# Optimization experiments

Hardware: AMD Instinct MI355X
Metric: run time of the kernel (lower is better)

Reference implementation:

```python
import jax, jax.numpy as jnp
import numpy as np

T, B = 512, 64
DIM_INPUT, DIM_LATENT, VOCAB = 512, 1024, 50257


def setup_inputs() -> dict:
    key = jax.random.key(0)
    ks = jax.random.split(key, 12)
    s = 0.02
    return {
        "X": jax.random.randint(ks[0], (T, B), 0, VOCAB, dtype=jnp.int32),
        "h": jax.random.normal(ks[1], (B, DIM_LATENT), dtype=jnp.float32),
        "emb": jax.random.normal(ks[2], (VOCAB, DIM_INPUT), dtype=jnp.float32) * s,
        "Wf": jax.random.normal(ks[3], (DIM_LATENT + DIM_INPUT, DIM_LATENT), dtype=jnp.float32) * s,
        "bf": jnp.zeros((DIM_LATENT,), dtype=jnp.float32),
        "Wi": jax.random.normal(ks[4], (DIM_LATENT + DIM_INPUT, DIM_LATENT), dtype=jnp.float32) * s,
        "bi": jnp.zeros((DIM_LATENT,), dtype=jnp.float32),
        "Wc": jax.random.normal(ks[5], (DIM_LATENT + DIM_INPUT, DIM_LATENT), dtype=jnp.float32) * s,
        "bc": jnp.zeros((DIM_LATENT,), dtype=jnp.float32),
        "Wo": jax.random.normal(ks[6], (DIM_LATENT + DIM_INPUT, DIM_LATENT), dtype=jnp.float32) * s,
        "bo": jnp.zeros((DIM_LATENT,), dtype=jnp.float32),
    }


def reference(X, h, emb, Wf, bf, Wi, bi, Wc, bc, Wo, bo):
    # X: [T, B] int tokens; h: [B, dim_latent]
    xe = emb[X]  # [T, B, dim_input] embedding gather
    c0 = jnp.zeros_like(h)

    def step(carry, x_t):
        h_prev, c_prev = carry
        m = jnp.concatenate([h_prev, x_t], axis=1)  # [B, dl+di]
        ft = jax.nn.sigmoid(m @ Wf + bf)
        it = jax.nn.sigmoid(m @ Wi + bi)
        ct = ft * c_prev + it * jnp.tanh(m @ Wc + bc)
        ot = jax.nn.sigmoid(m @ Wo + bo)
        ht = ot * jnp.tanh(ct)
        return (ht, ct), ht

    (_, _), H = jax.lax.scan(step, (h, c0), xe)
    return H  # [T, B, dim_latent]
```

## Files before the change

### kernel.cpp

```cpp
#include <hip/hip_runtime.h>


namespace {
constexpr int T_STEPS = 512;
constexpr int BATCH   = 64;
constexpr int DI      = 512;
constexpr int DL      = 1024;
constexpr int NKC     = 48;
constexpr int NKC_H   = 32;
constexpr int NBLK    = 256;
constexpr int NTHR    = 256;
constexpr int FPAD    = 32;
}

typedef __attribute__((ext_vector_type(8))) short bf16x8;
typedef __attribute__((ext_vector_type(8))) unsigned short u16x8;
typedef __attribute__((ext_vector_type(4))) float f32x4;
typedef __attribute__((ext_vector_type(4))) unsigned int u32x4;
typedef __attribute__((ext_vector_type(2))) unsigned int u32x2;

__device__ __forceinline__ unsigned short f2bf(float x){
  unsigned int u = __float_as_uint(x);
  return (unsigned short)((u + 0x7FFFu + ((u >> 16) & 1u)) >> 16);
}
__device__ __forceinline__ float bf2f(unsigned short b){
  return __uint_as_float(((unsigned int)b) << 16);
}
__device__ __forceinline__ float fast_sigmoid(float v){
  return __fdividef(1.f, 1.f + __expf(-v));
}
__device__ __forceinline__ float fast_tanh(float v){
  v = fminf(fmaxf(v, -15.f), 15.f);
  float t = __expf(2.f * v);
  return __fdividef(t - 1.f, t + 1.f);
}

__global__ void prep_xe(const int* __restrict__ X, const float* __restrict__ emb,
                        unsigned short* __restrict__ xe){
  int i = blockIdx.x * blockDim.x + threadIdx.x;
  const int total = T_STEPS * BATCH * DI / 8;
  if (i >= total) return;
  int row = i >> 6;
  int seg = i & 63;
  int tok = X[row];
  const float* src = emb + (long long)tok * DI + seg * 8;
  float4 v0 = *(const float4*)src;
  float4 v1 = *(const float4*)(src + 4);
  u16x8 o;
  o[0]=f2bf(v0.x); o[1]=f2bf(v0.y); o[2]=f2bf(v0.z); o[3]=f2bf(v0.w);
  o[4]=f2bf(v1.x); o[5]=f2bf(v1.y); o[6]=f2bf(v1.z); o[7]=f2bf(v1.w);
  *(u16x8*)(xe + (long long)row * DI + seg * 8) = o;
}

__global__ void prep_w(const float* __restrict__ Wf, const float* __restrict__ Wi,
                       const float* __restrict__ Wc, const float* __restrict__ Wo,
                       unsigned short* __restrict__ W_hi, unsigned short* __restrict__ W_lo){
  int idx = blockIdx.x * blockDim.x + threadIdx.x;
  if (idx >= 256 * NKC * 64) return;
  int lane = idx & 63;
  int kc   = (idx >> 6) % NKC;
  int bk   = idx / (64 * NKC);
  int lc = lane & 15, kg = lane >> 4;
  int g  = lc >> 2;
  int jl = bk * 4 + (lc & 3);
  const float* Wg = (g == 0) ? Wf : ((g == 1) ? Wi : ((g == 2) ? Wc : Wo));
  int kbase = kc * 32 + kg * 8;
  u16x8 hi, lo;
#pragma unroll
  for (int j = 0; j < 8; j++){
    float wv = Wg[(long long)(kbase + j) * DL + jl];
    unsigned short h = f2bf(wv);
    hi[j] = h;
    lo[j] = f2bf(wv - bf2f(h));
  }
  *(u16x8*)(W_hi + ((long long)(bk * NKC + kc) * 64 + lane) * 8) = hi;
  if (kc < NKC_H)
    *(u16x8*)(W_lo + ((long long)(bk * NKC_H + kc) * 64 + lane) * 8) = lo;
}

__global__ void prep_h(const float* __restrict__ h0,
                       const float* __restrict__ bf_, const float* __restrict__ bi_,
                       const float* __restrict__ bc_, const float* __restrict__ bo_,
                       unsigned short* __restrict__ hRing,
                       float* __restrict__ bias_pack, unsigned int* __restrict__ bar){
  int i = blockIdx.x * blockDim.x + threadIdx.x;
  if (i < BATCH * DL) hRing[i] = f2bf(h0[i]);
  if (i < 4096){
    int r = i & 3, g = (i >> 2) & 3, bk = i >> 4;
    const float* bg = (g == 0) ? bf_ : ((g == 1) ? bi_ : ((g == 2) ? bc_ : bo_));
    bias_pack[i] = bg[bk * 4 + r];
  }
  if (i < 8 * FPAD) bar[i] = 0u;
}

template<bool CACHED>
__launch_bounds__(NTHR, 1)
__global__ void lstm_persist(const unsigned short* __restrict__ xe,
                             const unsigned short* __restrict__ W_hi,
                             const unsigned short* __restrict__ W_lo,
                             unsigned short* __restrict__ hRing,
                             const float* __restrict__ bias_pack,
                             float* __restrict__ out,
                             unsigned int* __restrict__ bar){
  extern __shared__ unsigned short lds[];
  unsigned short* lds_hi = lds;
  unsigned short* lds_lo = lds + NKC * 512;
  __shared__ unsigned short stage_h[BATCH * 4];
  __shared__ float          stage_o[BATCH * 4];
  const int tid  = threadIdx.x;
  const int bk   = blockIdx.x;
  const int w    = tid >> 6;
  const int lane = tid & 63;

  const uint4* srcHi = (const uint4*)(W_hi + (size_t)bk * NKC * 512);
  uint4* dHi = (uint4*)lds_hi;
  for (int i = tid; i < 3072; i += NTHR) dHi[i] = srcHi[i];
  const uint4* srcLo = (const uint4*)(W_lo + (size_t)bk * NKC_H * 512);
  uint4* dLo = (uint4*)lds_lo;
  for (int i = tid; i < 2048; i += NTHR) dLo[i] = srcLo[i];
  __syncthreads();

  const int lc = lane & 15;
  const int kg = lane >> 4;
  const int g  = lc >> 2;
  const int rowb = (w << 4) + lc;
  const float bias = bias_pack[bk * 16 + lc];
  const int srcBase = (lane & 48) | (lc & 3);
  const int hOff = rowb * DL + kg * 8;
  const int xOff = rowb * DI + kg * 8;
  float cr0 = 0.f, cr1 = 0.f, cr2 = 0.f, cr3 = 0.f;

  f32x4 acc0 = {0.f,0.f,0.f,0.f}, acc1 = {0.f,0.f,0.f,0.f};
  f32x4 acc2 = {0.f,0.f,0.f,0.f}, acc3 = {0.f,0.f,0.f,0.f};

#define XSTEP(KC, ACC) {                                                        \
    bf16x8 ax = *(const bf16x8*)(xRow + (KC) * 32);                             \
    bf16x8 bh = *(const bf16x8*)(lds_hi + (NKC_H + (KC)) * 512 + lane * 8);     \
    ACC = __builtin_amdgcn_mfma_f32_16x16x32_bf16(ax, bh, ACC, 0, 0, 0); }
#define HSTEP2(KC, ACC) {                                                       \
    bf16x8 ah = *(const bf16x8*)&hv[KC];                                        \
    bf16x8 bh = *(const bf16x8*)(lds_hi + (KC) * 512 + lane * 8);               \
    bf16x8 bl = *(const bf16x8*)(lds_lo + (KC) * 512 + lane * 8);               \
    ACC = __builtin_amdgcn_mfma_f32_16x16x32_bf16(ah, bh, ACC, 0, 0, 0);        \
    ACC = __builtin_amdgcn_mfma_f32_16x16x32_bf16(ah, bl, ACC, 0, 0, 0); }
#define LOADHC(I, OFFSTR)                                                       \
    asm volatile("global_load_dwordx4 %0, %1, off offset:" OFFSTR               \
                 : "=v"(hv[I]) : "v"(hbase));
#define LOADHU(I, OFFSTR)                                                       \
    asm volatile("global_load_dwordx4 %0, %1, off offset:" OFFSTR " sc0 sc1"    \
                 : "=v"(hv[I]) : "v"(hbase));

  {
    const unsigned short* xRow = xe + xOff;
#pragma unroll
    for (int kc = 0; kc < 16; kc += 4){
      XSTEP(kc, acc0) XSTEP(kc + 1, acc1) XSTEP(kc + 2, acc2) XSTEP(kc + 3, acc3)
    }
  }

#pragma unroll 1
  for (int t = 0; t < T_STEPS; ++t){
    if (t > 0 && w == 0){
      const unsigned tgt = (unsigned)NBLK * (unsigned)t;
      int spin = 0;
      while (__hip_atomic_load(bar, __ATOMIC_RELAXED, __HIP_MEMORY_SCOPE_AGENT) < tgt){
        __builtin_amdgcn_s_sleep(1);
        if (++spin > (1 << 16)) break;
      }
    }
    __syncthreads();

    const int slotR = CACHED ? t       : (t & 1);
    const int slotW = CACHED ? (t + 1) : ((t + 1) & 1);
    unsigned short* hWr = hRing + (size_t)slotW * (BATCH * DL);
    float* out_t = out + (size_t)t * (BATCH * DL);

    u32x4 hv[32];
    const unsigned short* hbase = hRing + (size_t)slotR * (BATCH * DL) + hOff;
    if constexpr (CACHED){
      LOADHC( 0,"0")    LOADHC( 1,"64")   LOADHC( 2,"128")  LOADHC( 3,"192")
      LOADHC( 4,"256")  LOADHC( 5,"320")  LOADHC( 6,"384")  LOADHC( 7,"448")
      LOADHC( 8,"512")  LOADHC( 9,"576")  LOADHC(10,"640")  LOADHC(11,"704")
      LOADHC(12,"768")  LOADHC(13,"832")  LOADHC(14,"896")  LOADHC(15,"960")
      LOADHC(16,"1024") LOADHC(17,"1088") LOADHC(18,"1152") LOADHC(19,"1216")
      LOADHC(20,"1280") LOADHC(21,"1344") LOADHC(22,"1408") LOADHC(23,"1472")
      LOADHC(24,"1536") LOADHC(25,"1600") LOADHC(26,"1664") LOADHC(27,"1728")
      LOADHC(28,"1792") LOADHC(29,"1856") LOADHC(30,"1920") LOADHC(31,"1984")
    } else {
      LOADHU( 0,"0")    LOADHU( 1,"64")   LOADHU( 2,"128")  LOADHU( 3,"192")
      LOADHU( 4,"256")  LOADHU( 5,"320")  LOADHU( 6,"384")  LOADHU( 7,"448")
      LOADHU( 8,"512")  LOADHU( 9,"576")  LOADHU(10,"640")  LOADHU(11,"704")
      LOADHU(12,"768")  LOADHU(13,"832")  LOADHU(14,"896")  LOADHU(15,"960")
      LOADHU(16,"1024") LOADHU(17,"1088") LOADHU(18,"1152") LOADHU(19,"1216")
      LOADHU(20,"1280") LOADHU(21,"1344") LOADHU(22,"1408") LOADHU(23,"1472")
      LOADHU(24,"1536") LOADHU(25,"1600") LOADHU(26,"1664") LOADHU(27,"1728")
      LOADHU(28,"1792") LOADHU(29,"1856") LOADHU(30,"1920") LOADHU(31,"1984")
    }
    asm volatile("s_waitcnt vmcnt(0)" ::: "memory");
    __builtin_amdgcn_sched_barrier(0);

#pragma unroll
    for (int kc = 0; kc < NKC_H; kc += 4){
      HSTEP2(kc, acc0) HSTEP2(kc + 1, acc1) HSTEP2(kc + 2, acc2) HSTEP2(kc + 3, acc3)
    }
    f32x4 acc = (acc0 + acc1) + (acc2 + acc3);

    float creg[4] = {cr0, cr1, cr2, cr3};
#pragma unroll
    for (int r = 0; r < 4; r++){
      float v = acc[r] + bias;
      float vF = __shfl(v, srcBase);
      float vI = __shfl(v, srcBase + 4);
      float vC = __shfl(v, srcBase + 8);
      float vO = __shfl(v, srcBase + 12);
      if (g == 0){
        int b = (w << 4) | (kg << 2) | r;
        float ft = fast_sigmoid(vF);
        float it = fast_sigmoid(vI);
        float gt = fast_tanh(vC);
        float ot = fast_sigmoid(vO);
        float cn = ft * creg[r] + it * gt;
        creg[r] = cn;
        float hn = ot * fast_tanh(cn);
        int si = (b << 2) | (lc & 3);
        stage_h[si] = f2bf(hn);
        stage_o[si] = hn;
      }
    }
    cr0 = creg[0]; cr1 = creg[1]; cr2 = creg[2]; cr3 = creg[3];

    __syncthreads();

    if (w == 0){
      u32x2  hv2 = *(const u32x2*)&stage_h[lane << 2];
      f32x4  ov  = *(const f32x4*)&stage_o[lane << 2];
      *(float4*)(out_t + lane * DL + (bk << 2)) = *(const float4*)&ov;
      unsigned short* hdst = hWr + lane * DL + (bk << 2);
      asm volatile("global_store_dwordx2 %0, %1, off sc0 sc1"
                   :: "v"(hdst), "v"(hv2) : "memory");
      asm volatile("s_waitcnt vmcnt(0)" ::: "memory");
      __builtin_amdgcn_sched_barrier(0);
      if (tid == 0)
        __hip_atomic_fetch_add(bar, 1u, __ATOMIC_RELAXED, __HIP_MEMORY_SCOPE_AGENT);
    }

    acc0 = (f32x4){0.f,0.f,0.f,0.f}; acc1 = (f32x4){0.f,0.f,0.f,0.f};
    acc2 = (f32x4){0.f,0.f,0.f,0.f}; acc3 = (f32x4){0.f,0.f,0.f,0.f};
    if (t + 1 < T_STEPS){
      const unsigned short* xRow = xe + (size_t)(t + 1) * BATCH * DI + xOff;
#pragma unroll
      for (int kc = 0; kc < 16; kc += 4){
        XSTEP(kc, acc0) XSTEP(kc + 1, acc1) XSTEP(kc + 2, acc2) XSTEP(kc + 3, acc3)
      }
    }
  }
#undef XSTEP
#undef HSTEP2
#undef LOADHC
#undef LOADHU
}

extern "C" void kernel_launch(void* const* d_in, const int* in_sizes, int n_in,
                              void* d_out, int out_size, void* d_ws, size_t ws_size,
                              hipStream_t stream){
  const int*   X   = (const int*)d_in[0];
  const float* h0  = (const float*)d_in[1];
  const float* emb = (const float*)d_in[2];
  const float* Wf  = (const float*)d_in[3];
  const float* bf_ = (const float*)d_in[4];
  const float* Wi  = (const float*)d_in[5];
  const float* bi_ = (const float*)d_in[6];
  const float* Wc  = (const float*)d_in[7];
  const float* bc_ = (const float*)d_in[8];
  const float* Wo  = (const float*)d_in[9];
  const float* bo_ = (const float*)d_in[10];
  float* out = (float*)d_out;

  const size_t SLOT = (size_t)BATCH * DL;
  const size_t base_need =
      sizeof(unsigned short) * ((size_t)T_STEPS * BATCH * DI
                              + (size_t)256 * NKC * 512
                              + (size_t)256 * NKC_H * 512)
    + sizeof(float) * 4096
    + sizeof(unsigned int) * 8 * FPAD + 4096;
  const size_t ring_full = sizeof(unsigned short) * SLOT * (size_t)(T_STEPS + 1);
  const bool cached = ws_size >= base_need + ring_full;
  const size_t ring_elems = cached ? SLOT * (size_t)(T_STEPS + 1) : SLOT * 2;

  char* ws = (char*)d_ws;
  size_t off = 0;
  auto alloc = [&](size_t bytes) -> void* {
    void* p = ws + off;
    off = (off + bytes + 255) & ~((size_t)255);
    return p;
  };
  unsigned short* xe        = (unsigned short*)alloc(sizeof(unsigned short) * (size_t)T_STEPS * BATCH * DI);
  unsigned short* W_hi      = (unsigned short*)alloc(sizeof(unsigned short) * (size_t)256 * NKC * 512);
  unsigned short* W_lo      = (unsigned short*)alloc(sizeof(unsigned short) * (size_t)256 * NKC_H * 512);
  unsigned short* hRing     = (unsigned short*)alloc(sizeof(unsigned short) * ring_elems);
  float*          bias_pack = (float*)alloc(sizeof(float) * 4096);
  unsigned int*   bar       = (unsigned int*)alloc(sizeof(unsigned int) * 8 * FPAD);
  (void)in_sizes; (void)n_in; (void)out_size;

  static bool attr_set = false;
  if (!attr_set){
    hipFuncSetAttribute((const void*)lstm_persist<true>,
                        hipFuncAttributeMaxDynamicSharedMemorySize, 160 * 1024);
    hipFuncSetAttribute((const void*)lstm_persist<false>,
                        hipFuncAttributeMaxDynamicSharedMemorySize, 160 * 1024);
    attr_set = true;
  }

  hipLaunchKernelGGL(prep_xe, dim3(8192), dim3(256), 0, stream, X, emb, xe);
  hipLaunchKernelGGL(prep_w,  dim3(3072), dim3(256), 0, stream, Wf, Wi, Wc, Wo, W_hi, W_lo);
  hipLaunchKernelGGL(prep_h,  dim3(256),  dim3(256), 0, stream, h0, bf_, bi_, bc_, bo_,
                     hRing, bias_pack, bar);
  if (cached)
    hipLaunchKernelGGL((lstm_persist<true>),  dim3(NBLK), dim3(NTHR), 80 * 1024, stream,
                       xe, W_hi, W_lo, hRing, bias_pack, out, bar);
  else
    hipLaunchKernelGGL((lstm_persist<false>), dim3(NBLK), dim3(NTHR), 80 * 1024, stream,
                       xe, W_hi, W_lo, hRing, bias_pack, out, bar);
}
```

Measured before the change: 4.905 ms.

## Replace global atomic barrier with sentinel-polled h ring for step sync

The per-step global atomic counter barrier and the block-wide syncthreads are replaced by dataflow synchronization. The whole h ring is pre-filled with a sentinel value, and each wave issues its h loads for the next step early, then re-polls only the chunks that still hold sentinel values until valid data arrives. Each wave now writes its own outputs directly instead of staging them through wave 0. This removes the all-block barrier latency and lets waves proceed as soon as their data is ready. In exchange it adds a full-ring fill kernel, requires a full-length ring in the workspace with no fallback, relies on torn 16-byte visibility being caught by a partial sentinel check, and uses a spin cap that could silently read stale data.

After: 8.863 ms. +80.7%, slower.

```diff
diff --git a/kernel.cpp b/kernel.cpp
--- a/kernel.cpp
+++ b/kernel.cpp
@@ -10,7 +10,7 @@
 constexpr int NKC_H   = 32;
 constexpr int NBLK    = 256;
 constexpr int NTHR    = 256;
-constexpr int FPAD    = 32;
+constexpr unsigned SENT = 0xFFFFFFFFu;
 }
 
 typedef __attribute__((ext_vector_type(8))) short bf16x8;
@@ -33,6 +33,11 @@
   v = fminf(fmaxf(v, -15.f), 15.f);
   float t = __expf(2.f * v);
   return __fdividef(t - 1.f, t + 1.f);
+}
+
+__global__ void prep_ring(u32x4* __restrict__ dst, int n16){
+  int i = blockIdx.x * blockDim.x + threadIdx.x;
+  if (i < n16) dst[i] = (u32x4){SENT, SENT, SENT, SENT};
 }
 
 __global__ void prep_xe(const int* __restrict__ X, const float* __restrict__ emb,
@@ -82,7 +87,7 @@
                        const float* __restrict__ bf_, const float* __restrict__ bi_,
                        const float* __restrict__ bc_, const float* __restrict__ bo_,
                        unsigned short* __restrict__ hRing,
-                       float* __restrict__ bias_pack, unsigned int* __restrict__ bar){
+                       float* __restrict__ bias_pack){
   int i = blockIdx.x * blockDim.x + threadIdx.x;
   if (i < BATCH * DL) hRing[i] = f2bf(h0[i]);
   if (i < 4096){
@@ -90,23 +95,20 @@
     const float* bg = (g == 0) ? bf_ : ((g == 1) ? bi_ : ((g == 2) ? bc_ : bo_));
     bias_pack[i] = bg[bk * 4 + r];
   }
-  if (i < 8 * FPAD) bar[i] = 0u;
-}
-
-template<bool CACHED>
+}
+
 __launch_bounds__(NTHR, 1)
 __global__ void lstm_persist(const unsigned short* __restrict__ xe,
                              const unsigned short* __restrict__ W_hi,
                              const unsigned short* __restrict__ W_lo,
                              unsigned short* __restrict__ hRing,
                              const float* __restrict__ bias_pack,
-                             float* __restrict__ out,
-                             unsigned int* __restrict__ bar){
+                             float* __restrict__ out){
   extern __shared__ unsigned short lds[];
   unsigned short* lds_hi = lds;
   unsigned short* lds_lo = lds + NKC * 512;
-  __shared__ unsigned short stage_h[BATCH * 4];
-  __shared__ float          stage_o[BATCH * 4];
+  __shared__ __align__(8)  unsigned short sh_h[4][64];
+  __shared__ __align__(16) float          sh_o[4][64];
   const int tid  = threadIdx.x;
   const int bk   = blockIdx.x;
   const int w    = tid >> 6;
@@ -132,6 +134,7 @@
 
   f32x4 acc0 = {0.f,0.f,0.f,0.f}, acc1 = {0.f,0.f,0.f,0.f};
   f32x4 acc2 = {0.f,0.f,0.f,0.f}, acc3 = {0.f,0.f,0.f,0.f};
+  u32x4 hv[32];
 
 #define XSTEP(KC, ACC) {                                                        \
     bf16x8 ax = *(const bf16x8*)(xRow + (KC) * 32);                             \
@@ -143,14 +146,28 @@
     bf16x8 bl = *(const bf16x8*)(lds_lo + (KC) * 512 + lane * 8);               \
     ACC = __builtin_amdgcn_mfma_f32_16x16x32_bf16(ah, bh, ACC, 0, 0, 0);        \
     ACC = __builtin_amdgcn_mfma_f32_16x16x32_bf16(ah, bl, ACC, 0, 0, 0); }
-#define LOADHC(I, OFFSTR)                                                       \
-    asm volatile("global_load_dwordx4 %0, %1, off offset:" OFFSTR               \
-                 : "=v"(hv[I]) : "v"(hbase));
 #define LOADHU(I, OFFSTR)                                                       \
     asm volatile("global_load_dwordx4 %0, %1, off offset:" OFFSTR " sc0 sc1"    \
                  : "=v"(hv[I]) : "v"(hbase));
+#define ISSUE_ALL                                                               \
+    LOADHU( 0,"0")    LOADHU( 1,"64")   LOADHU( 2,"128")  LOADHU( 3,"192")     \
+    LOADHU( 4,"256")  LOADHU( 5,"320")  LOADHU( 6,"384")  LOADHU( 7,"448")     \
+    LOADHU( 8,"512")  LOADHU( 9,"576")  LOADHU(10,"640")  LOADHU(11,"704")     \
+    LOADHU(12,"768")  LOADHU(13,"832")  LOADHU(14,"896")  LOADHU(15,"960")     \
+    LOADHU(16,"1024") LOADHU(17,"1088") LOADHU(18,"1152") LOADHU(19,"1216")    \
+    LOADHU(20,"1280") LOADHU(21,"1344") LOADHU(22,"1408") LOADHU(23,"1472")    \
+    LOADHU(24,"1536") LOADHU(25,"1600") LOADHU(26,"1664") LOADHU(27,"1728")    \
+    LOADHU(28,"1792") LOADHU(29,"1856") LOADHU(30,"1920") LOADHU(31,"1984")
+#define CHK(KC) { int bad = (hv[KC][0] == SENT) | (hv[KC][2] == SENT);          \
+                  if (__any(bad)) inval |= (1u << (KC)); }
+#define RLD(KC, OFFSTR) if (inval & (1u << (KC))) { LOADHU(KC, OFFSTR) }
+#define RCK(KC) if (inval & (1u << (KC))) {                                     \
+                  int bad = (hv[KC][0] == SENT) | (hv[KC][2] == SENT);          \
+                  if (!__any(bad)) inval &= ~(1u << (KC)); }
 
   {
+    const unsigned short* hbase = hRing + hOff;
+    ISSUE_ALL
     const unsigned short* xRow = xe + xOff;
 #pragma unroll
     for (int kc = 0; kc < 16; kc += 4){
@@ -160,44 +177,35 @@
 
 #pragma unroll 1
   for (int t = 0; t < T_STEPS; ++t){
-    if (t > 0 && w == 0){
-      const unsigned tgt = (unsigned)NBLK * (unsigned)t;
-      int spin = 0;
-      while (__hip_atomic_load(bar, __ATOMIC_RELAXED, __HIP_MEMORY_SCOPE_AGENT) < tgt){
-        __builtin_amdgcn_s_sleep(1);
-        if (++spin > (1 << 16)) break;
-      }
-    }
-    __syncthreads();
-
-    const int slotR = CACHED ? t       : (t & 1);
-    const int slotW = CACHED ? (t + 1) : ((t + 1) & 1);
-    unsigned short* hWr = hRing + (size_t)slotW * (BATCH * DL);
-    float* out_t = out + (size_t)t * (BATCH * DL);
-
-    u32x4 hv[32];
-    const unsigned short* hbase = hRing + (size_t)slotR * (BATCH * DL) + hOff;
-    if constexpr (CACHED){
-      LOADHC( 0,"0")    LOADHC( 1,"64")   LOADHC( 2,"128")  LOADHC( 3,"192")
-      LOADHC( 4,"256")  LOADHC( 5,"320")  LOADHC( 6,"384")  LOADHC( 7,"448")
-      LOADHC( 8,"512")  LOADHC( 9,"576")  LOADHC(10,"640")  LOADHC(11,"704")
-      LOADHC(12,"768")  LOADHC(13,"832")  LOADHC(14,"896")  LOADHC(15,"960")
-      LOADHC(16,"1024") LOADHC(17,"1088") LOADHC(18,"1152") LOADHC(19,"1216")
-      LOADHC(20,"1280") LOADHC(21,"1344") LOADHC(22,"1408") LOADHC(23,"1472")
-      LOADHC(24,"1536") LOADHC(25,"1600") LOADHC(26,"1664") LOADHC(27,"1728")
-      LOADHC(28,"1792") LOADHC(29,"1856") LOADHC(30,"1920") LOADHC(31,"1984")
-    } else {
-      LOADHU( 0,"0")    LOADHU( 1,"64")   LOADHU( 2,"128")  LOADHU( 3,"192")
-      LOADHU( 4,"256")  LOADHU( 5,"320")  LOADHU( 6,"384")  LOADHU( 7,"448")
-      LOADHU( 8,"512")  LOADHU( 9,"576")  LOADHU(10,"640")  LOADHU(11,"704")
-      LOADHU(12,"768")  LOADHU(13,"832")  LOADHU(14,"896")  LOADHU(15,"960")
-      LOADHU(16,"1024") LOADHU(17,"1088") LOADHU(18,"1152") LOADHU(19,"1216")
-      LOADHU(20,"1280") LOADHU(21,"1344") LOADHU(22,"1408") LOADHU(23,"1472")
-      LOADHU(24,"1536") LOADHU(25,"1600") LOADHU(26,"1664") LOADHU(27,"1728")
-      LOADHU(28,"1792") LOADHU(29,"1856") LOADHU(30,"1920") LOADHU(31,"1984")
-    }
     asm volatile("s_waitcnt vmcnt(0)" ::: "memory");
     __builtin_amdgcn_sched_barrier(0);
+    unsigned inval = 0u;
+    CHK( 0) CHK( 1) CHK( 2) CHK( 3) CHK( 4) CHK( 5) CHK( 6) CHK( 7)
+    CHK( 8) CHK( 9) CHK(10) CHK(11) CHK(12) CHK(13) CHK(14) CHK(15)
+    CHK(16) CHK(17) CHK(18) CHK(19) CHK(20) CHK(21) CHK(22) CHK(23)
+    CHK(24) CHK(25) CHK(26) CHK(27) CHK(28) CHK(29) CHK(30) CHK(31)
+    if (inval){
+      const unsigned short* hbase = hRing + (size_t)t * (BATCH * DL) + hOff;
+      int spin = 0;
+      do {
+        __builtin_amdgcn_s_sleep(1);
+        RLD( 0,"0")    RLD( 1,"64")   RLD( 2,"128")  RLD( 3,"192")
+        RLD( 4,"256")  RLD( 5,"320")  RLD( 6,"384")  RLD( 7,"448")
+        RLD( 8,"512")  RLD( 9,"576")  RLD(10,"640")  RLD(11,"704")
+        RLD(12,"768")  RLD(13,"832")  RLD(14,"896")  RLD(15,"960")
+        RLD(16,"1024") RLD(17,"1088") RLD(18,"1152") RLD(19,"1216")
+        RLD(20,"1280") RLD(21,"1344") RLD(22,"1408") RLD(23,"1472")
+        RLD(24,"1536") RLD(25,"1600") RLD(26,"1664") RLD(27,"1728")
+        RLD(28,"1792") RLD(29,"1856") RLD(30,"1920") RLD(31,"1984")
+        asm volatile("s_waitcnt vmcnt(0)" ::: "memory");
+        __builtin_amdgcn_sched_barrier(0);
+        RCK( 0) RCK( 1) RCK( 2) RCK( 3) RCK( 4) RCK( 5) RCK( 6) RCK( 7)
+        RCK( 8) RCK( 9) RCK(10) RCK(11) RCK(12) RCK(13) RCK(14) RCK(15)
+        RCK(16) RCK(17) RCK(18) RCK(19) RCK(20) RCK(21) RCK(22) RCK(23)
+        RCK(24) RCK(25) RCK(26) RCK(27) RCK(28) RCK(29) RCK(30) RCK(31)
+        if (++spin > (1 << 15)) break;
+      } while (inval);
+    }
 
 #pragma unroll
     for (int kc = 0; kc < NKC_H; kc += 4){
@@ -214,7 +222,6 @@
       float vC = __shfl(v, srcBase + 8);
       float vO = __shfl(v, srcBase + 12);
       if (g == 0){
-        int b = (w << 4) | (kg << 2) | r;
         float ft = fast_sigmoid(vF);
         float it = fast_sigmoid(vI);
         float gt = fast_tanh(vC);
@@ -222,31 +229,31 @@
         float cn = ft * creg[r] + it * gt;
         creg[r] = cn;
         float hn = ot * fast_tanh(cn);
-        int si = (b << 2) | (lc & 3);
-        stage_h[si] = f2bf(hn);
-        stage_o[si] = hn;
+        int si = ((kg << 2) | r) * 4 + (lc & 3);
+        sh_h[w][si] = f2bf(hn);
+        sh_o[w][si] = hn;
       }
     }
     cr0 = creg[0]; cr1 = creg[1]; cr2 = creg[2]; cr3 = creg[3];
 
-    __syncthreads();
-
-    if (w == 0){
-      u32x2  hv2 = *(const u32x2*)&stage_h[lane << 2];
-      f32x4  ov  = *(const f32x4*)&stage_o[lane << 2];
-      *(float4*)(out_t + lane * DL + (bk << 2)) = *(const float4*)&ov;
-      unsigned short* hdst = hWr + lane * DL + (bk << 2);
+    asm volatile("s_waitcnt lgkmcnt(0)" ::: "memory");
+    __builtin_amdgcn_sched_barrier(0);
+
+    if (lane < 16){
+      int row = (w << 4) + lane;
+      u32x2  hv2 = *(const u32x2*)&sh_h[w][lane << 2];
+      float4 ov  = *(const float4*)&sh_o[w][lane << 2];
+      *(float4*)(out + (size_t)t * (BATCH * DL) + row * DL + (bk << 2)) = ov;
+      unsigned short* hdst = hRing + (size_t)(t + 1) * (BATCH * DL) + row * DL + (bk << 2);
       asm volatile("global_store_dwordx2 %0, %1, off sc0 sc1"
                    :: "v"(hdst), "v"(hv2) : "memory");
-      asm volatile("s_waitcnt vmcnt(0)" ::: "memory");
-      __builtin_amdgcn_sched_barrier(0);
-      if (tid == 0)
-        __hip_atomic_fetch_add(bar, 1u, __ATOMIC_RELAXED, __HIP_MEMORY_SCOPE_AGENT);
     }
 
     acc0 = (f32x4){0.f,0.f,0.f,0.f}; acc1 = (f32x4){0.f,0.f,0.f,0.f};
     acc2 = (f32x4){0.f,0.f,0.f,0.f}; acc3 = (f32x4){0.f,0.f,0.f,0.f};
     if (t + 1 < T_STEPS){
+      const unsigned short* hbase = hRing + (size_t)(t + 1) * (BATCH * DL) + hOff;
+      ISSUE_ALL
       const unsigned short* xRow = xe + (size_t)(t + 1) * BATCH * DI + xOff;
 #pragma unroll
       for (int kc = 0; kc < 16; kc += 4){
@@ -256,8 +263,11 @@
   }
 #undef XSTEP
 #undef HSTEP2
-#undef LOADHC
 #undef LOADHU
+#undef ISSUE_ALL
+#undef CHK
+#undef RLD
+#undef RCK
 }
 
 extern "C" void kernel_launch(void* const* d_in, const int* in_sizes, int n_in,
@@ -277,15 +287,7 @@
   float* out = (float*)d_out;
 
   const size_t SLOT = (size_t)BATCH * DL;
-  const size_t base_need =
-      sizeof(unsigned short) * ((size_t)T_STEPS * BATCH * DI
-                              + (size_t)256 * NKC * 512
-                              + (size_t)256 * NKC_H * 512)
-    + sizeof(float) * 4096
-    + sizeof(unsigned int) * 8 * FPAD + 4096;
-  const size_t ring_full = sizeof(unsigned short) * SLOT * (size_t)(T_STEPS + 1);
-  const bool cached = ws_size >= base_need + ring_full;
-  const size_t ring_elems = cached ? SLOT * (size_t)(T_STEPS + 1) : SLOT * 2;
+  const size_t ring_elems = SLOT * (size_t)(T_STEPS + 1);
 
   char* ws = (char*)d_ws;
   size_t off = 0;
@@ -299,26 +301,22 @@
   unsigned short* W_lo      = (unsigned short*)alloc(sizeof(unsigned short) * (size_t)256 * NKC_H * 512);
   unsigned short* hRing     = (unsigned short*)alloc(sizeof(unsigned short) * ring_elems);
   float*          bias_pack = (float*)alloc(sizeof(float) * 4096);
-  unsigned int*   bar       = (unsigned int*)alloc(sizeof(unsigned int) * 8 * FPAD);
-  (void)in_sizes; (void)n_in; (void)out_size;
+  (void)in_sizes; (void)n_in; (void)out_size; (void)ws_size;
 
   static bool attr_set = false;
   if (!attr_set){
-    hipFuncSetAttribute((const void*)lstm_persist<true>,
-                        hipFuncAttributeMaxDynamicSharedMemorySize, 160 * 1024);
-    hipFuncSetAttribute((const void*)lstm_persist<false>,
+    hipFuncSetAttribute((const void*)lstm_persist,
                         hipFuncAttributeMaxDynamicSharedMemorySize, 160 * 1024);
     attr_set = true;
   }
 
+  const int n16 = (int)((ring_elems * 2 + 15) / 16);
+  hipLaunchKernelGGL(prep_ring, dim3((n16 + 255) / 256), dim3(256), 0, stream,
+                     (u32x4*)hRing, n16);
   hipLaunchKernelGGL(prep_xe, dim3(8192), dim3(256), 0, stream, X, emb, xe);
   hipLaunchKernelGGL(prep_w,  dim3(3072), dim3(256), 0, stream, Wf, Wi, Wc, Wo, W_hi, W_lo);
   hipLaunchKernelGGL(prep_h,  dim3(256),  dim3(256), 0, stream, h0, bf_, bi_, bc_, bo_,
-                     hRing, bias_pack, bar);
-  if (cached)
-    hipLaunchKernelGGL((lstm_persist<true>),  dim3(NBLK), dim3(NTHR), 80 * 1024, stream,
-                       xe, W_hi, W_lo, hRing, bias_pack, out, bar);
-  else
-    hipLaunchKernelGGL((lstm_persist<false>), dim3(NBLK), dim3(NTHR), 80 * 1024, stream,
-                       xe, W_hi, W_lo, hRing, bias_pack, out, bar);
-}
+                     hRing, bias_pack);
+  hipLaunchKernelGGL(lstm_persist, dim3(NBLK), dim3(NTHR), 80 * 1024, stream,
+                     xe, W_hi, W_lo, hRing, bias_pack, out);
+}
```
